# Performance work log

Measured on AMD Instinct MI355X. Metric: run time of the kernel, lower is better.

Reference implementation:

```python
import jax, jax.numpy as jnp
import numpy as np

D, H, DFF, MD = 1024, 16, 4096, 128
B, TS, TT = 8, 512, 512
EPS = 1e-6


def _ln(x, s, b):
    m = jnp.mean(x, axis=-1, keepdims=True)
    v = jnp.mean((x - m) ** 2, axis=-1, keepdims=True)
    return (x - m) * jax.lax.rsqrt(v + EPS) * s + b


def _rel_bias(emb, qlen, klen):
    # T5-style bidirectional bucket: [H, qlen, klen]
    q = jnp.arange(qlen)[:, None]
    k = jnp.arange(klen)[None, :]
    rp = k - q
    bucket = jnp.where(rp < 0, jnp.minimum(-rp, MD - 1), jnp.minimum(rp, MD - 1) + MD)
    return emb[bucket].transpose(2, 0, 1)


def _mha(xq, xkv, w_in, b_in, w_out, b_out, bias):
    # nn.MultiheadAttention math: packed in_proj [3D,D], additive attn bias [H,Tq,Tk]
    Bq, Tq, _ = xq.shape
    Tk = xkv.shape[1]
    hd = D // H
    wq, wk, wv = jnp.split(w_in, 3, axis=0)
    bq, bk, bv = jnp.split(b_in, 3, axis=0)
    q = (xq @ wq.T + bq).reshape(Bq, Tq, H, hd).transpose(0, 2, 1, 3)
    k = (xkv @ wk.T + bk).reshape(Bq, Tk, H, hd).transpose(0, 2, 1, 3)
    v = (xkv @ wv.T + bv).reshape(Bq, Tk, H, hd).transpose(0, 2, 1, 3)
    scores = jnp.einsum('bhqd,bhkd->bhqk', q, k) / jnp.sqrt(jnp.asarray(hd, xq.dtype))
    scores = scores + bias[None]
    attn = jax.nn.softmax(scores, axis=-1)
    out = jnp.einsum('bhqk,bhkd->bhqd', attn, v)
    out = out.transpose(0, 2, 1, 3).reshape(Bq, Tq, D)
    return out @ w_out.T + b_out


def setup_inputs() -> dict:
    key = jax.random.key(0)
    ks = jax.random.split(key, 40)
    std = 0.02

    def n(i, shape):
        return jax.random.normal(ks[i], shape, dtype=jnp.float32) * std

    return {
        'src': jax.random.normal(ks[0], (B, TS, D), dtype=jnp.float32),
        'tgt': jax.random.normal(ks[1], (B, TT, D), dtype=jnp.float32),
        # encoder layer
        'enc_in_w': n(2, (3 * D, D)), 'enc_in_b': jnp.zeros((3 * D,)),
        'enc_out_w': n(3, (D, D)), 'enc_out_b': jnp.zeros((D,)),
        'enc_ff1_w': n(4, (DFF, D)), 'enc_ff1_b': jnp.zeros((DFF,)),
        'enc_ff2_w': n(5, (D, DFF)), 'enc_ff2_b': jnp.zeros((D,)),
        'enc_n1_s': jnp.ones((D,)), 'enc_n1_b': jnp.zeros((D,)),
        'enc_n2_s': jnp.ones((D,)), 'enc_n2_b': jnp.zeros((D,)),
        'enc_rel': n(6, (2 * MD, H)),
        # decoder layer
        'dec_sa_in_w': n(7, (3 * D, D)), 'dec_sa_in_b': jnp.zeros((3 * D,)),
        'dec_sa_out_w': n(8, (D, D)), 'dec_sa_out_b': jnp.zeros((D,)),
        'dec_ca_in_w': n(9, (3 * D, D)), 'dec_ca_in_b': jnp.zeros((3 * D,)),
        'dec_ca_out_w': n(10, (D, D)), 'dec_ca_out_b': jnp.zeros((D,)),
        'dec_ff1_w': n(11, (DFF, D)), 'dec_ff1_b': jnp.zeros((DFF,)),
        'dec_ff2_w': n(12, (D, DFF)), 'dec_ff2_b': jnp.zeros((D,)),
        'dec_n1_s': jnp.ones((D,)), 'dec_n1_b': jnp.zeros((D,)),
        'dec_n2_s': jnp.ones((D,)), 'dec_n2_b': jnp.zeros((D,)),
        'dec_n3_s': jnp.ones((D,)), 'dec_n3_b': jnp.zeros((D,)),
        'dec_rel_self': n(13, (2 * MD, H)),
        'dec_rel_cross': n(14, (2 * MD, H)),
    }


def reference(src, tgt,
              enc_in_w, enc_in_b, enc_out_w, enc_out_b,
              enc_ff1_w, enc_ff1_b, enc_ff2_w, enc_ff2_b,
              enc_n1_s, enc_n1_b, enc_n2_s, enc_n2_b, enc_rel,
              dec_sa_in_w, dec_sa_in_b, dec_sa_out_w, dec_sa_out_b,
              dec_ca_in_w, dec_ca_in_b, dec_ca_out_w, dec_ca_out_b,
              dec_ff1_w, dec_ff1_b, dec_ff2_w, dec_ff2_b,
              dec_n1_s, dec_n1_b, dec_n2_s, dec_n2_b, dec_n3_s, dec_n3_b,
              dec_rel_self, dec_rel_cross):
    Ts, Tt = src.shape[1], tgt.shape[1]

    # ---- encoder layer (pre-LN) ----
    eb = _rel_bias(enc_rel, Ts, Ts)  # [H,Ts,Ts]
    x = src
    x = x + _mha(_ln(x, enc_n1_s, enc_n1_b), _ln(x, enc_n1_s, enc_n1_b),
                 enc_in_w, enc_in_b, enc_out_w, enc_out_b, eb)
    h = _ln(x, enc_n2_s, enc_n2_b)
    x = x + (jax.nn.relu(h @ enc_ff1_w.T + enc_ff1_b) @ enc_ff2_w.T + enc_ff2_b)
    memory = x

    # ---- decoder layer (pre-LN) ----
    causal = jnp.where(jnp.arange(Tt)[None, :] > jnp.arange(Tt)[:, None], -jnp.inf, 0.0)
    sb = _rel_bias(dec_rel_self, Tt, Tt) + causal[None]  # [H,Tt,Tt]
    cb = _rel_bias(dec_rel_cross, Tt, Ts)                # [H,Tt,Ts]
    y = tgt
    yn = _ln(y, dec_n1_s, dec_n1_b)
    y = y + _mha(yn, yn, dec_sa_in_w, dec_sa_in_b, dec_sa_out_w, dec_sa_out_b, sb)
    y = y + _mha(_ln(y, dec_n2_s, dec_n2_b), memory,
                 dec_ca_in_w, dec_ca_in_b, dec_ca_out_w, dec_ca_out_b, cb)
    h = _ln(y, dec_n3_s, dec_n3_b)
    y = y + (jax.nn.relu(h @ dec_ff1_w.T + dec_ff1_b) @ dec_ff2_w.T + dec_ff2_b)
    return y
```

## Files before the change

kernel.cpp:

```cpp
#include <hip/hip_runtime.h>

using u16 = unsigned short;

typedef float f32x4 __attribute__((ext_vector_type(4)));
typedef __bf16 bf16x8v __attribute__((ext_vector_type(8)));
typedef bf16x8v bf16x8 __attribute__((may_alias));
typedef u16 u16x8v __attribute__((ext_vector_type(8)));
typedef u16x8v u16x8 __attribute__((may_alias));
typedef u16 u16x4v __attribute__((ext_vector_type(4)));
typedef u16x4v u16x4 __attribute__((may_alias));
typedef float f32x4v __attribute__((ext_vector_type(4)));
typedef f32x4v float4a __attribute__((may_alias));

#define GPTR(p) ((__attribute__((address_space(1))) void*)(p))
#define LPTR(p) ((__attribute__((address_space(3))) void*)(p))

__device__ __forceinline__ u16 f2bf(float f) {
  unsigned u = __builtin_bit_cast(unsigned, f);
  u += 0x7FFFu + ((u >> 16) & 1u);
  return (u16)(u >> 16);
}

__device__ __forceinline__ f32x4 mfma16(bf16x8 a, bf16x8 b, f32x4 c) {
  return __builtin_amdgcn_mfma_f32_16x16x32_bf16(a, b, c, 0, 0, 0);
}

__global__ __launch_bounds__(256) void cvt_bf16(const float* __restrict__ in,
                                                u16* __restrict__ out, int n4) {
  int i = blockIdx.x * 256 + threadIdx.x;
  if (i < n4) {
    float4a v = ((const float4a*)in)[i];
    u16x4 o;
    o[0] = f2bf(v[0]); o[1] = f2bf(v[1]); o[2] = f2bf(v[2]); o[3] = f2bf(v[3]);
    ((u16x4*)out)[i] = o;
  }
}

__global__ __launch_bounds__(256) void ln_k(const float* __restrict__ x,
                                            const float* __restrict__ sc,
                                            const float* __restrict__ bi,
                                            u16* __restrict__ out) {
  const int row = blockIdx.x, tid = threadIdx.x;
  float4a v = ((const float4a*)(x + (size_t)row * 1024))[tid];
  float s1 = v[0] + v[1] + v[2] + v[3];
  float s2 = v[0]*v[0] + v[1]*v[1] + v[2]*v[2] + v[3]*v[3];
#pragma unroll
  for (int off = 32; off; off >>= 1) { s1 += __shfl_xor(s1, off); s2 += __shfl_xor(s2, off); }
  __shared__ float red[8];
  if ((tid & 63) == 0) { red[tid >> 6] = s1; red[4 + (tid >> 6)] = s2; }
  __syncthreads();
  s1 = red[0] + red[1] + red[2] + red[3];
  s2 = red[4] + red[5] + red[6] + red[7];
  const float mean = s1 * (1.f / 1024.f);
  const float rstd = rsqrtf(s2 * (1.f / 1024.f) - mean * mean + 1e-6f);
  float4a s4 = ((const float4a*)sc)[tid];
  float4a b4 = ((const float4a*)bi)[tid];
  u16x4 o;
#pragma unroll
  for (int j = 0; j < 4; j++) o[j] = f2bf((v[j] - mean) * rstd * s4[j] + b4[j]);
  ((u16x4*)(out + (size_t)row * 1024))[tid] = o;
}

template <int BN_T, int MW, int EPI>
__global__ __launch_bounds__(256) void gemm_bt(
    const u16* __restrict__ A, int lda,
    const u16* __restrict__ W, int ldw,
    const float* __restrict__ bias,
    const float* __restrict__ C0, int ldc0,
    void* __restrict__ outv, int ldo, int K) {
  constexpr int BM = 128, BK = 64;
  constexpr int NW = 4 / MW;
  constexpr int FM = BM / MW / 16;
  constexpr int FN = BN_T / NW / 16;
  constexpr int RA = (BM * BK * 2) / 4096;
  constexpr int RB = (BN_T * BK * 2) / 4096;
  __shared__ alignas(16) u16 As[BM * BK];
  __shared__ alignas(16) u16 Bs[BN_T * BK];
  const int tid = threadIdx.x, lane = tid & 63, wv = tid >> 6;
  const int bm = blockIdx.y * BM, bn = blockIdx.x * BN_T;
  const int wr = (wv / NW) * (BM / MW);
  const int wc = (wv % NW) * (BN_T / NW);
  const int la = lane & 15, lk = (lane >> 4) * 8;
  const int srow = wv * 8 + (lane >> 3), scol = (lane & 7) * 8;
  const u16* gA = A + (size_t)(bm + srow) * lda + scol;
  const u16* gB = W + (size_t)(bn + srow) * ldw + scol;
  u16* lA = As + (wv * 8) * BK;
  u16* lB = Bs + (wv * 8) * BK;

  f32x4 acc[FM][FN] = {};

  for (int k0 = 0; k0 < K; k0 += BK) {
    __syncthreads();
#pragma unroll
    for (int r = 0; r < RA; r++)
      __builtin_amdgcn_global_load_lds(GPTR(gA + (size_t)r * 32 * lda + k0),
                                       LPTR(lA + r * 32 * BK), 16, 0, 0);
#pragma unroll
    for (int r = 0; r < RB; r++)
      __builtin_amdgcn_global_load_lds(GPTR(gB + (size_t)r * 32 * ldw + k0),
                                       LPTR(lB + r * 32 * BK), 16, 0, 0);
    __syncthreads();
#pragma unroll
    for (int kk = 0; kk < BK; kk += 32) {
      bf16x8 af[FM], bfr[FN];
#pragma unroll
      for (int m = 0; m < FM; m++) af[m] = *(const bf16x8*)&As[(wr + m * 16 + la) * BK + kk + lk];
#pragma unroll
      for (int n = 0; n < FN; n++) bfr[n] = *(const bf16x8*)&Bs[(wc + n * 16 + la) * BK + kk + lk];
#pragma unroll
      for (int m = 0; m < FM; m++)
#pragma unroll
        for (int n = 0; n < FN; n++)
          acc[m][n] = mfma16(af[m], bfr[n], acc[m][n]);
    }
  }
  float bv[FN];
#pragma unroll
  for (int n = 0; n < FN; n++) bv[n] = bias[bn + wc + n * 16 + la];
#pragma unroll
  for (int m = 0; m < FM; m++) {
#pragma unroll
    for (int j = 0; j < 4; j++) {
      const int row = bm + wr + m * 16 + (lane >> 4) * 4 + j;
#pragma unroll
      for (int n = 0; n < FN; n++) {
        const int col = bn + wc + n * 16 + la;
        float v = acc[m][n][j] + bv[n];
        if constexpr (EPI == 1) v = fmaxf(v, 0.f);
        if constexpr (EPI == 2) {
          ((float*)outv)[(size_t)row * ldo + col] = v + C0[(size_t)row * ldc0 + col];
        } else {
          ((u16*)outv)[(size_t)row * ldo + col] = f2bf(v);
        }
      }
    }
  }
}

template <bool CAUSAL>
__global__ __launch_bounds__(256) void attn_k(
    const u16* __restrict__ Qb, int ldq,
    const u16* __restrict__ Kb, int ldk,
    const u16* __restrict__ Vb, int ldv,
    const float* __restrict__ rel,
    u16* __restrict__ Ob, int ldo,
    int Tq, int Tk) {
  __shared__ alignas(16) u16 Ks[128][72];
  __shared__ alignas(16) u16 Vt[64][136];
  __shared__ alignas(16) u16 Ps[4][16][136];
  __shared__ float biasl[256];
  const int tid = threadIdx.x, lane = tid & 63, w = tid >> 6;
  const int b = blockIdx.y >> 4, h = blockIdx.y & 15;
  const int q0 = blockIdx.x * 64;
  const int la = lane & 15, lg = lane >> 4;

  biasl[tid] = rel[tid * 16 + h];

  const int qr0 = q0 + w * 16;
  const u16* qp = Qb + (size_t)(b * Tq + qr0 + la) * ldq + h * 64 + lg * 8;
  const bf16x8 qf0 = *(const bf16x8*)qp;
  const bf16x8 qf1 = *(const bf16x8*)(qp + 32);

  float m[4], sm[4];
  f32x4 acc[4] = {};
#pragma unroll
  for (int j = 0; j < 4; j++) { m[j] = -1e30f; sm[j] = 0.f; }

  const int kv_end = CAUSAL ? (q0 + 64) : Tk;
  const int srow = tid >> 3, scol = (tid & 7) * 8;
  for (int kv0 = 0; kv0 < kv_end; kv0 += 128) {
    __syncthreads();
#pragma unroll
    for (int r = 0; r < 4; r++) {
      const int row = r * 32 + srow;
      const size_t gr = (size_t)(b * Tk + kv0 + row);
      *(u16x8*)&Ks[row][scol] = *(const u16x8*)&Kb[gr * ldk + h * 64 + scol];
      u16x8 vv = *(const u16x8*)&Vb[gr * ldv + h * 64 + scol];
#pragma unroll
      for (int j = 0; j < 8; j++) Vt[scol + j][row] = vv[j];
    }
    __syncthreads();

    f32x4 s[8];
#pragma unroll
    for (int kvt = 0; kvt < 8; kvt++) {
      const bf16x8 kf0 = *(const bf16x8*)&Ks[kvt * 16 + la][lg * 8];
      const bf16x8 kf1 = *(const bf16x8*)&Ks[kvt * 16 + la][32 + lg * 8];
      f32x4 t = {};
      t = mfma16(qf0, kf0, t);
      t = mfma16(qf1, kf1, t);
      const int kc = kv0 + kvt * 16 + la;
#pragma unroll
      for (int j = 0; j < 4; j++) {
        const int qr = qr0 + lg * 4 + j;
        const int rp = kc - qr;
        const int bucket = rp < 0 ? (rp > -127 ? -rp : 127) : (rp < 127 ? rp : 127) + 128;
        float sv = t[j] * 0.125f + biasl[bucket];
        if (CAUSAL && kc > qr) sv = -1e30f;
        s[kvt][j] = sv;
      }
    }
    float alpha[4];
#pragma unroll
    for (int j = 0; j < 4; j++) {
      float tm = s[0][j];
#pragma unroll
      for (int kvt = 1; kvt < 8; kvt++) tm = fmaxf(tm, s[kvt][j]);
#pragma unroll
      for (int off = 1; off < 16; off <<= 1) tm = fmaxf(tm, __shfl_xor(tm, off));
      const float mn = fmaxf(m[j], tm);
      alpha[j] = __expf(m[j] - mn);
      m[j] = mn;
      float r = 0.f;
#pragma unroll
      for (int kvt = 0; kvt < 8; kvt++) {
        const float p = __expf(s[kvt][j] - mn);
        s[kvt][j] = p;
        r += p;
      }
#pragma unroll
      for (int off = 1; off < 16; off <<= 1) r += __shfl_xor(r, off);
      sm[j] = sm[j] * alpha[j] + r;
    }
#pragma unroll
    for (int kvt = 0; kvt < 8; kvt++)
#pragma unroll
      for (int j = 0; j < 4; j++)
        Ps[w][lg * 4 + j][kvt * 16 + la] = f2bf(s[kvt][j]);
#pragma unroll
    for (int n = 0; n < 4; n++)
#pragma unroll
      for (int j = 0; j < 4; j++)
        acc[n][j] *= alpha[j];
#pragma unroll
    for (int kq = 0; kq < 4; kq++) {
      const bf16x8 pf = *(const bf16x8*)&Ps[w][la][kq * 32 + lg * 8];
#pragma unroll
      for (int n = 0; n < 4; n++) {
        const bf16x8 vf = *(const bf16x8*)&Vt[n * 16 + la][kq * 32 + lg * 8];
        acc[n] = mfma16(pf, vf, acc[n]);
      }
    }
  }
#pragma unroll
  for (int n = 0; n < 4; n++)
#pragma unroll
    for (int j = 0; j < 4; j++) {
      const int qr = qr0 + lg * 4 + j;
      Ob[(size_t)(b * Tq + qr) * ldo + h * 64 + n * 16 + la] = f2bf(acc[n][j] / sm[j]);
    }
}

extern "C" void kernel_launch(void* const* d_in, const int* in_sizes, int n_in,
                              void* d_out, int out_size, void* d_ws, size_t ws_size,
                              hipStream_t stream) {
  (void)in_sizes; (void)n_in; (void)out_size; (void)ws_size;
  const float* src       = (const float*)d_in[0];
  const float* tgt       = (const float*)d_in[1];
  const float* enc_in_w  = (const float*)d_in[2];
  const float* enc_in_b  = (const float*)d_in[3];
  const float* enc_out_w = (const float*)d_in[4];
  const float* enc_out_b = (const float*)d_in[5];
  const float* enc_ff1_w = (const float*)d_in[6];
  const float* enc_ff1_b = (const float*)d_in[7];
  const float* enc_ff2_w = (const float*)d_in[8];
  const float* enc_ff2_b = (const float*)d_in[9];
  const float* enc_n1_s  = (const float*)d_in[10];
  const float* enc_n1_b  = (const float*)d_in[11];
  const float* enc_n2_s  = (const float*)d_in[12];
  const float* enc_n2_b  = (const float*)d_in[13];
  const float* enc_rel   = (const float*)d_in[14];
  const float* dsa_in_w  = (const float*)d_in[15];
  const float* dsa_in_b  = (const float*)d_in[16];
  const float* dsa_out_w = (const float*)d_in[17];
  const float* dsa_out_b = (const float*)d_in[18];
  const float* dca_in_w  = (const float*)d_in[19];
  const float* dca_in_b  = (const float*)d_in[20];
  const float* dca_out_w = (const float*)d_in[21];
  const float* dca_out_b = (const float*)d_in[22];
  const float* dff1_w    = (const float*)d_in[23];
  const float* dff1_b    = (const float*)d_in[24];
  const float* dff2_w    = (const float*)d_in[25];
  const float* dff2_b    = (const float*)d_in[26];
  const float* dn1_s     = (const float*)d_in[27];
  const float* dn1_b     = (const float*)d_in[28];
  const float* dn2_s     = (const float*)d_in[29];
  const float* dn2_b     = (const float*)d_in[30];
  const float* dn3_s     = (const float*)d_in[31];
  const float* dn3_b     = (const float*)d_in[32];
  const float* drel_s    = (const float*)d_in[33];
  const float* drel_c    = (const float*)d_in[34];
  float* fo = (float*)d_out;

  char* w8 = (char*)d_ws;
  float* x_ws  = (float*)(w8 + 0);
  u16* ln_buf  = (u16*)(w8 + 16777216);
  u16* qkv     = (u16*)(w8 + 25165824);
  u16* attn_o  = (u16*)(w8 + 50331648);
  u16* ffh     = qkv;
  u16* memb    = (u16*)(w8 + 58720256);
  u16* wb      = (u16*)(w8 + 67108864);

  u16* w_enc_in  = wb;
  u16* w_enc_out = wb + 3145728;
  u16* w_enc_f1  = wb + 4194304;
  u16* w_enc_f2  = wb + 8388608;
  u16* w_dsa_in  = wb + 12582912;
  u16* w_dsa_out = wb + 15728640;
  u16* w_dca_in  = wb + 16777216;
  u16* w_dca_out = wb + 19922944;
  u16* w_dff1    = wb + 20971520;
  u16* w_dff2    = wb + 25165824;

#define CVT(sp, dp, n) cvt_bf16<<<dim3((n) / 1024), 256, 0, stream>>>(sp, dp, (n) / 4)
  CVT(enc_in_w,  w_enc_in,  3145728);
  CVT(enc_out_w, w_enc_out, 1048576);
  CVT(enc_ff1_w, w_enc_f1,  4194304);
  CVT(enc_ff2_w, w_enc_f2,  4194304);
  CVT(dsa_in_w,  w_dsa_in,  3145728);
  CVT(dsa_out_w, w_dsa_out, 1048576);
  CVT(dca_in_w,  w_dca_in,  3145728);
  CVT(dca_out_w, w_dca_out, 1048576);
  CVT(dff1_w,    w_dff1,    4194304);
  CVT(dff2_w,    w_dff2,    4194304);
#undef CVT

  ln_k<<<dim3(4096), 256, 0, stream>>>(src, enc_n1_s, enc_n1_b, ln_buf);
  gemm_bt<128,2,0><<<dim3(24, 32), 256, 0, stream>>>(ln_buf, 1024, w_enc_in, 1024, enc_in_b, nullptr, 0, qkv, 3072, 1024);
  attn_k<false><<<dim3(8, 128), 256, 0, stream>>>(qkv, 3072, qkv + 1024, 3072, qkv + 2048, 3072, enc_rel, attn_o, 1024, 512, 512);
  gemm_bt<64,4,2><<<dim3(16, 32), 256, 0, stream>>>(attn_o, 1024, w_enc_out, 1024, enc_out_b, src, 1024, x_ws, 1024, 1024);
  ln_k<<<dim3(4096), 256, 0, stream>>>(x_ws, enc_n2_s, enc_n2_b, ln_buf);
  gemm_bt<128,2,1><<<dim3(32, 32), 256, 0, stream>>>(ln_buf, 1024, w_enc_f1, 1024, enc_ff1_b, nullptr, 0, ffh, 4096, 1024);
  gemm_bt<64,4,2><<<dim3(16, 32), 256, 0, stream>>>(ffh, 4096, w_enc_f2, 4096, enc_ff2_b, x_ws, 1024, x_ws, 1024, 4096);
  cvt_bf16<<<dim3(4096), 256, 0, stream>>>(x_ws, memb, 1048576);

  ln_k<<<dim3(4096), 256, 0, stream>>>(tgt, dn1_s, dn1_b, ln_buf);
  gemm_bt<128,2,0><<<dim3(24, 32), 256, 0, stream>>>(ln_buf, 1024, w_dsa_in, 1024, dsa_in_b, nullptr, 0, qkv, 3072, 1024);
  attn_k<true><<<dim3(8, 128), 256, 0, stream>>>(qkv, 3072, qkv + 1024, 3072, qkv + 2048, 3072, drel_s, attn_o, 1024, 512, 512);
  gemm_bt<64,4,2><<<dim3(16, 32), 256, 0, stream>>>(attn_o, 1024, w_dsa_out, 1024, dsa_out_b, tgt, 1024, fo, 1024, 1024);

  ln_k<<<dim3(4096), 256, 0, stream>>>(fo, dn2_s, dn2_b, ln_buf);
  gemm_bt<64,4,0><<<dim3(16, 32), 256, 0, stream>>>(ln_buf, 1024, w_dca_in, 1024, dca_in_b, nullptr, 0, qkv, 3072, 1024);
  gemm_bt<128,2,0><<<dim3(16, 32), 256, 0, stream>>>(memb, 1024, w_dca_in + 1048576, 1024, dca_in_b + 1024, nullptr, 0, qkv + 1024, 3072, 1024);
  attn_k<false><<<dim3(8, 128), 256, 0, stream>>>(qkv, 3072, qkv + 1024, 3072, qkv + 2048, 3072, drel_c, attn_o, 1024, 512, 512);
  gemm_bt<64,4,2><<<dim3(16, 32), 256, 0, stream>>>(attn_o, 1024, w_dca_out, 1024, dca_out_b, fo, 1024, fo, 1024, 1024);

  ln_k<<<dim3(4096), 256, 0, stream>>>(fo, dn3_s, dn3_b, ln_buf);
  gemm_bt<128,2,1><<<dim3(32, 32), 256, 0, stream>>>(ln_buf, 1024, w_dff1, 1024, dff1_b, nullptr, 0, ffh, 4096, 1024);
  gemm_bt<64,4,2><<<dim3(16, 32), 256, 0, stream>>>(ffh, 4096, w_dff2, 4096, dff2_b, fo, 1024, fo, 1024, 4096);
}
```

Before: 703.6 us.

## Double-buffer GEMM LDS tiles, swizzle LDS layout, and remap workgroups across XCDs

Adds a PF template flag that double-buffers the A/B LDS tiles so the next K-slice's global-to-LDS loads overlap the MFMA compute on the current slice, with one waitcnt+barrier per stage. It also XOR-swizzles the 16-byte column chunks in LDS to cut bank conflicts on fragment reads. Workgroup IDs are remapped so consecutive tiles land on the same XCD, for better L2 reuse. Double buffering is enabled only for the BN=64 GEMMs, which doubles their LDS footprint and may reduce occupancy.

New measurement: 674.1 us. 1.04x faster.

```diff
diff --git a/kernel.cpp b/kernel.cpp
--- a/kernel.cpp
+++ b/kernel.cpp
@@ -24,6 +24,13 @@
 __device__ __forceinline__ f32x4 mfma16(bf16x8 a, bf16x8 b, f32x4 c) {
   return __builtin_amdgcn_mfma_f32_16x16x32_bf16(a, b, c, 0, 0, 0);
 }
+
+#define WAITBAR()                                          \
+  do {                                                     \
+    asm volatile("s_waitcnt vmcnt(0)" ::: "memory");       \
+    __builtin_amdgcn_s_barrier();                          \
+    __builtin_amdgcn_sched_barrier(0);                     \
+  } while (0)
 
 __global__ __launch_bounds__(256) void cvt_bf16(const float* __restrict__ in,
                                                 u16* __restrict__ out, int n4) {
@@ -61,7 +68,7 @@
   ((u16x4*)(out + (size_t)row * 1024))[tid] = o;
 }
 
-template <int BN_T, int MW, int EPI>
+template <int BN_T, int MW, int EPI, int PF>
 __global__ __launch_bounds__(256) void gemm_bt(
     const u16* __restrict__ A, int lda,
     const u16* __restrict__ W, int ldw,
@@ -74,46 +81,84 @@
   constexpr int FN = BN_T / NW / 16;
   constexpr int RA = (BM * BK * 2) / 4096;
   constexpr int RB = (BN_T * BK * 2) / 4096;
-  __shared__ alignas(16) u16 As[BM * BK];
-  __shared__ alignas(16) u16 Bs[BN_T * BK];
+  constexpr int NB = PF ? 2 : 1;
+  __shared__ alignas(16) u16 As[NB][BM * BK];
+  __shared__ alignas(16) u16 Bs[NB][BN_T * BK];
   const int tid = threadIdx.x, lane = tid & 63, wv = tid >> 6;
-  const int bm = blockIdx.y * BM, bn = blockIdx.x * BN_T;
+
+  const int gx = gridDim.x;
+  const int nwg = gx * gridDim.y;
+  const int orig = blockIdx.y * gx + blockIdx.x;
+  const int qq = nwg >> 3, rr = nwg & 7;
+  const int xcd = orig & 7, idx = orig >> 3;
+  const int wg = (xcd < rr ? xcd * (qq + 1) : rr * (qq + 1) + (xcd - rr) * qq) + idx;
+  const int bm = (wg / gx) * BM, bn = (wg % gx) * BN_T;
+
   const int wr = (wv / NW) * (BM / MW);
   const int wc = (wv % NW) * (BN_T / NW);
-  const int la = lane & 15, lk = (lane >> 4) * 8;
-  const int srow = wv * 8 + (lane >> 3), scol = (lane & 7) * 8;
+  const int la = lane & 15, lg = lane >> 4;
+  const int r7 = la & 7;
+  const int srow = wv * 8 + (lane >> 3);
+  const int scol = ((lane & 7) ^ (lane >> 3)) << 3;
   const u16* gA = A + (size_t)(bm + srow) * lda + scol;
   const u16* gB = W + (size_t)(bn + srow) * ldw + scol;
-  u16* lA = As + (wv * 8) * BK;
-  u16* lB = Bs + (wv * 8) * BK;
 
   f32x4 acc[FM][FN] = {};
 
-  for (int k0 = 0; k0 < K; k0 += BK) {
-    __syncthreads();
-#pragma unroll
-    for (int r = 0; r < RA; r++)
-      __builtin_amdgcn_global_load_lds(GPTR(gA + (size_t)r * 32 * lda + k0),
-                                       LPTR(lA + r * 32 * BK), 16, 0, 0);
-#pragma unroll
-    for (int r = 0; r < RB; r++)
-      __builtin_amdgcn_global_load_lds(GPTR(gB + (size_t)r * 32 * ldw + k0),
-                                       LPTR(lB + r * 32 * BK), 16, 0, 0);
-    __syncthreads();
-#pragma unroll
-    for (int kk = 0; kk < BK; kk += 32) {
-      bf16x8 af[FM], bfr[FN];
-#pragma unroll
-      for (int m = 0; m < FM; m++) af[m] = *(const bf16x8*)&As[(wr + m * 16 + la) * BK + kk + lk];
-#pragma unroll
-      for (int n = 0; n < FN; n++) bfr[n] = *(const bf16x8*)&Bs[(wc + n * 16 + la) * BK + kk + lk];
-#pragma unroll
-      for (int m = 0; m < FM; m++)
-#pragma unroll
-        for (int n = 0; n < FN; n++)
-          acc[m][n] = mfma16(af[m], bfr[n], acc[m][n]);
+#define STAGE(buf, k0)                                                              \
+  do {                                                                              \
+    _Pragma("unroll")                                                               \
+    for (int r = 0; r < RA; r++)                                                    \
+      __builtin_amdgcn_global_load_lds(GPTR(gA + (size_t)r * 32 * lda + (k0)),      \
+                                       LPTR(&As[buf][(wv * 8 + r * 32) * BK]), 16, 0, 0); \
+    _Pragma("unroll")                                                               \
+    for (int r = 0; r < RB; r++)                                                    \
+      __builtin_amdgcn_global_load_lds(GPTR(gB + (size_t)r * 32 * ldw + (k0)),      \
+                                       LPTR(&Bs[buf][(wv * 8 + r * 32) * BK]), 16, 0, 0); \
+  } while (0)
+
+#define COMPUTE(buf)                                                                \
+  do {                                                                              \
+    _Pragma("unroll")                                                               \
+    for (int kk = 0; kk < BK; kk += 32) {                                           \
+      const int off = ((((kk >> 3) + lg) ^ r7) << 3);                               \
+      bf16x8 af[FM], bfr[FN];                                                       \
+      _Pragma("unroll")                                                             \
+      for (int m = 0; m < FM; m++)                                                  \
+        af[m] = *(const bf16x8*)&As[buf][(wr + m * 16 + la) * BK + off];            \
+      _Pragma("unroll")                                                             \
+      for (int n = 0; n < FN; n++)                                                  \
+        bfr[n] = *(const bf16x8*)&Bs[buf][(wc + n * 16 + la) * BK + off];           \
+      _Pragma("unroll")                                                             \
+      for (int m = 0; m < FM; m++)                                                  \
+        _Pragma("unroll")                                                           \
+        for (int n = 0; n < FN; n++)                                                \
+          acc[m][n] = mfma16(af[m], bfr[n], acc[m][n]);                             \
+    }                                                                               \
+  } while (0)
+
+  if constexpr (PF) {
+    STAGE(0, 0);
+    WAITBAR();
+    for (int k0 = 0; k0 < K; k0 += 2 * BK) {
+      STAGE(1, k0 + BK);
+      COMPUTE(0);
+      WAITBAR();
+      if (k0 + 2 * BK < K) STAGE(0, k0 + 2 * BK);
+      COMPUTE(1);
+      WAITBAR();
+    }
+  } else {
+    for (int k0 = 0; k0 < K; k0 += BK) {
+      __syncthreads();
+      STAGE(0, k0);
+      __syncthreads();
+      COMPUTE(0);
     }
   }
+#undef STAGE
+#undef COMPUTE
+
   float bv[FN];
 #pragma unroll
   for (int n = 0; n < FN; n++) bv[n] = bias[bn + wc + n * 16 + la];
@@ -326,26 +371,26 @@
 #undef CVT
 
   ln_k<<<dim3(4096), 256, 0, stream>>>(src, enc_n1_s, enc_n1_b, ln_buf);
-  gemm_bt<128,2,0><<<dim3(24, 32), 256, 0, stream>>>(ln_buf, 1024, w_enc_in, 1024, enc_in_b, nullptr, 0, qkv, 3072, 1024);
+  gemm_bt<128,2,0,0><<<dim3(24, 32), 256, 0, stream>>>(ln_buf, 1024, w_enc_in, 1024, enc_in_b, nullptr, 0, qkv, 3072, 1024);
   attn_k<false><<<dim3(8, 128), 256, 0, stream>>>(qkv, 3072, qkv + 1024, 3072, qkv + 2048, 3072, enc_rel, attn_o, 1024, 512, 512);
-  gemm_bt<64,4,2><<<dim3(16, 32), 256, 0, stream>>>(attn_o, 1024, w_enc_out, 1024, enc_out_b, src, 1024, x_ws, 1024, 1024);
+  gemm_bt<64,4,2,1><<<dim3(16, 32), 256, 0, stream>>>(attn_o, 1024, w_enc_out, 1024, enc_out_b, src, 1024, x_ws, 1024, 1024);
   ln_k<<<dim3(4096), 256, 0, stream>>>(x_ws, enc_n2_s, enc_n2_b, ln_buf);
-  gemm_bt<128,2,1><<<dim3(32, 32), 256, 0, stream>>>(ln_buf, 1024, w_enc_f1, 1024, enc_ff1_b, nullptr, 0, ffh, 4096, 1024);
-  gemm_bt<64,4,2><<<dim3(16, 32), 256, 0, stream>>>(ffh, 4096, w_enc_f2, 4096, enc_ff2_b, x_ws, 1024, x_ws, 1024, 4096);
+  gemm_bt<128,2,1,0><<<dim3(32, 32), 256, 0, stream>>>(ln_buf, 1024, w_enc_f1, 1024, enc_ff1_b, nullptr, 0, ffh, 4096, 1024);
+  gemm_bt<64,4,2,1><<<dim3(16, 32), 256, 0, stream>>>(ffh, 4096, w_enc_f2, 4096, enc_ff2_b, x_ws, 1024, x_ws, 1024, 4096);
   cvt_bf16<<<dim3(4096), 256, 0, stream>>>(x_ws, memb, 1048576);
 
   ln_k<<<dim3(4096), 256, 0, stream>>>(tgt, dn1_s, dn1_b, ln_buf);
-  gemm_bt<128,2,0><<<dim3(24, 32), 256, 0, stream>>>(ln_buf, 1024, w_dsa_in, 1024, dsa_in_b, nullptr, 0, qkv, 3072, 1024);
+  gemm_bt<128,2,0,0><<<dim3(24, 32), 256, 0, stream>>>(ln_buf, 1024, w_dsa_in, 1024, dsa_in_b, nullptr, 0, qkv, 3072, 1024);
   attn_k<true><<<dim3(8, 128), 256, 0, stream>>>(qkv, 3072, qkv + 1024, 3072, qkv + 2048, 3072, drel_s, attn_o, 1024, 512, 512);
-  gemm_bt<64,4,2><<<dim3(16, 32), 256, 0, stream>>>(attn_o, 1024, w_dsa_out, 1024, dsa_out_b, tgt, 1024, fo, 1024, 1024);
+  gemm_bt<64,4,2,1><<<dim3(16, 32), 256, 0, stream>>>(attn_o, 1024, w_dsa_out, 1024, dsa_out_b, tgt, 1024, fo, 1024, 1024);
 
   ln_k<<<dim3(4096), 256, 0, stream>>>(fo, dn2_s, dn2_b, ln_buf);
-  gemm_bt<64,4,0><<<dim3(16, 32), 256, 0, stream>>>(ln_buf, 1024, w_dca_in, 1024, dca_in_b, nullptr, 0, qkv, 3072, 1024);
-  gemm_bt<128,2,0><<<dim3(16, 32), 256, 0, stream>>>(memb, 1024, w_dca_in + 1048576, 1024, dca_in_b + 1024, nullptr, 0, qkv + 1024, 3072, 1024);
+  gemm_bt<64,4,0,1><<<dim3(16, 32), 256, 0, stream>>>(ln_buf, 1024, w_dca_in, 1024, dca_in_b, nullptr, 0, qkv, 3072, 1024);
+  gemm_bt<128,2,0,0><<<dim3(16, 32), 256, 0, stream>>>(memb, 1024, w_dca_in + 1048576, 1024, dca_in_b + 1024, nullptr, 0, qkv + 1024, 3072, 1024);
   attn_k<false><<<dim3(8, 128), 256, 0, stream>>>(qkv, 3072, qkv + 1024, 3072, qkv + 2048, 3072, drel_c, attn_o, 1024, 512, 512);
-  gemm_bt<64,4,2><<<dim3(16, 32), 256, 0, stream>>>(attn_o, 1024, w_dca_out, 1024, dca_out_b, fo, 1024, fo, 1024, 1024);
+  gemm_bt<64,4,2,1><<<dim3(16, 32), 256, 0, stream>>>(attn_o, 1024, w_dca_out, 1024, dca_out_b, fo, 1024, fo, 1024, 1024);
 
   ln_k<<<dim3(4096), 256, 0, stream>>>(fo, dn3_s, dn3_b, ln_buf);
-  gemm_bt<128,2,1><<<dim3(32, 32), 256, 0, stream>>>(ln_buf, 1024, w_dff1, 1024, dff1_b, nullptr, 0, ffh, 4096, 1024);
-  gemm_bt<64,4,2><<<dim3(16, 32), 256, 0, stream>>>(ffh, 4096, w_dff2, 4096, dff2_b, fo, 1024, fo, 1024, 4096);
-}
+  gemm_bt<128,2,1,0><<<dim3(32, 32), 256, 0, stream>>>(ln_buf, 1024, w_dff1, 1024, dff1_b, nullptr, 0, ffh, 4096, 1024);
+  gemm_bt<64,4,2,1><<<dim3(16, 32), 256, 0, stream>>>(ffh, 4096, w_dff2, 4096, dff2_b, fo, 1024, fo, 1024, 4096);
+}
```
